# Kernel optimization log

Hardware: AMD Instinct MI355X
Metric: run time of the kernel (lower is better)

Reference implementation:

```python
import jax, jax.numpy as jnp
import numpy as np
import math

B, S, D, H = 2, 2048, 1024, 16
DH = D // H  # head_dim = 64


def setup_inputs() -> dict:
    key = jax.random.key(0)
    k0, k1, k2 = jax.random.split(key, 3)
    x = jax.random.normal(k0, (B, S, D), dtype=jnp.float32)
    Wi = jax.random.normal(k1, (3 * D, D), dtype=jnp.float32) * 0.02  # torch (out,in) layout
    bi = jnp.zeros((3 * D,), dtype=jnp.float32)
    Wo = jax.random.normal(k2, (D, D), dtype=jnp.float32) * 0.02
    bo = jnp.zeros((D,), dtype=jnp.float32)
    return {"x": x, "Wi": Wi, "bi": bi, "Wo": Wo, "bo": bo, "causal_mask": 1}


def reference(x, Wi, bi, Wo, bo, causal_mask):
    b, s, d = x.shape
    # fused QKV projection: nn.Linear applies x @ W.T + b
    qkv = x @ Wi.T + bi                      # (b, s, 3d)
    q, k, v = jnp.split(qkv, 3, axis=-1)
    # (b, s, d) -> (b, h, s, dh)
    def to_heads(t):
        return t.reshape(b, s, H, DH).transpose(0, 2, 1, 3)
    q, k, v = to_heads(q), to_heads(k), to_heads(v)
    scores = jnp.einsum("bhqd,bhkd->bhqk", q, k)  # (b, h, s, s)
    if causal_mask:
        # mask strictly-upper triangle with -inf BEFORE scaling (as in source; -inf unaffected)
        tri = jnp.triu(jnp.ones((s, s), dtype=bool), k=1)
        scores = jnp.where(tri, -jnp.inf, scores)
    scores = scores / math.sqrt(DH)
    weight = jax.nn.softmax(scores, axis=-1)
    out = jnp.einsum("bhqk,bhkd->bhqd", weight, v)  # (b, h, s, dh)
    out = out.transpose(0, 2, 1, 3).reshape(b, s, d)
    return out @ Wo.T + bo
```

## Files before the change

### kernel.cpp

```cpp
#include <hip/hip_runtime.h>
#include <hip/hip_bf16.h>
#include <stdint.h>

#define B_    2
#define S_    2048
#define D_    1024
#define H_    16
#define DH_   64
#define MTOT  (B_*S_)
#define NQKV  (3*D_)

typedef __attribute__((ext_vector_type(8))) short  bf16x8;
typedef __attribute__((ext_vector_type(4))) short  bf16x4;
typedef __attribute__((ext_vector_type(4))) float  f32x4;
typedef __attribute__((ext_vector_type(8))) unsigned short u16x8;
typedef unsigned short ushort_t;

__device__ __forceinline__ ushort_t f2bf(float f) {
  union { float f; unsigned int i; } v; v.f = f;
  unsigned int r = v.i + 0x7FFF + ((v.i >> 16) & 1);
  return (ushort_t)(r >> 16);
}

__device__ __forceinline__ unsigned cvt_pk_bf16(float lo, float hi) {
  unsigned r;
  asm("v_cvt_pk_bf16_f32 %0, %1, %2" : "=v"(r) : "v"(lo), "v"(hi));
  return r;
}

__device__ __forceinline__ float fexp2(float x) {
  float r;
  asm("v_exp_f32 %0, %1" : "=v"(r) : "v"(x));
  return r;
}

#if __has_builtin(__builtin_amdgcn_mfma_f32_16x16x16_bf16)
__device__ __forceinline__ f32x4 mfma16(bf16x4 a, bf16x4 b, f32x4 c) {
  return __builtin_amdgcn_mfma_f32_16x16x16_bf16(a, b, c, 0, 0, 0);
}
#elif __has_builtin(__builtin_amdgcn_mfma_f32_16x16x16bf16_1k)
__device__ __forceinline__ f32x4 mfma16(bf16x4 a, bf16x4 b, f32x4 c) {
  return __builtin_amdgcn_mfma_f32_16x16x16bf16_1k(a, b, c, 0, 0, 0);
}
#else
__device__ __forceinline__ f32x4 mfma16(bf16x4 a, bf16x4 b, f32x4 c) {
  asm volatile("v_mfma_f32_16x16x16_bf16 %0, %1, %2, %0"
               : "+v"(c) : "v"(a), "v"(b));
  return c;
}
#endif

__device__ __forceinline__ void gl_lds16(const ushort_t* g, ushort_t* l) {
  __builtin_amdgcn_global_load_lds(
      (const __attribute__((address_space(1))) unsigned int*)g,
      (__attribute__((address_space(3))) unsigned int*)l, 16, 0, 0);
}

#define CVN1 (MTOT*D_/8)
#define CVN2 (NQKV*D_/8)
#define CVN3 (D_*D_/8)
__global__ __launch_bounds__(256) void cvt_all(
    const float* __restrict__ x, const float* __restrict__ Wi, const float* __restrict__ Wo,
    ushort_t* __restrict__ xb, ushort_t* __restrict__ Wib, ushort_t* __restrict__ Wob) {
  int i = blockIdx.x * blockDim.x + threadIdx.x;
  const float* src; ushort_t* dst; int k;
  if (i < CVN1)            { src = x;  dst = xb;  k = i; }
  else if (i < CVN1+CVN2)  { src = Wi; dst = Wib; k = i - CVN1; }
  else                     { src = Wo; dst = Wob; k = i - CVN1 - CVN2; }
  const float4* s4 = (const float4*)src;
  float4 a = s4[2*k], b = s4[2*k+1];
  u16x8 o;
  o[0]=f2bf(a.x); o[1]=f2bf(a.y); o[2]=f2bf(a.z); o[3]=f2bf(a.w);
  o[4]=f2bf(b.x); o[5]=f2bf(b.y); o[6]=f2bf(b.z); o[7]=f2bf(b.w);
  ((u16x8*)dst)[k] = o;
}

#define BKQ 32
#define BKO 64
#define QSCALE 0.18033688011112042f
__global__ __launch_bounds__(256) void gemm_qkv(
    const ushort_t* __restrict__ Abf, const ushort_t* __restrict__ Bbf,
    const float* __restrict__ bias,
    ushort_t* __restrict__ qb, ushort_t* __restrict__ kb, ushort_t* __restrict__ vb) {
  __shared__ __align__(16) ushort_t Al[128*BKQ];
  __shared__ __align__(16) ushort_t Bl[128*BKQ];
  int tid = threadIdx.x;
  int w = tid >> 6, lane = tid & 63;
  int wrow = (w >> 1) * 64, wcol = (w & 1) * 64;
  int m0 = blockIdx.y * 128, n0 = blockIdx.x * 128;
  const int K = D_;
  f32x4 zero = {0.f, 0.f, 0.f, 0.f};
  f32x4 acc[4][4];
  for (int i=0;i<4;i++) for (int j=0;j<4;j++) acc[i][j] = zero;

  for (int k0 = 0; k0 < K; k0 += BKQ) {
    __syncthreads();
    for (int it = 0; it < 2; ++it) {
      int c = it*256 + tid;
      int row = c >> 2, cc = c & 3;
      int lbase = (it*256 + w*64) * 8;
      gl_lds16(Abf + (size_t)(m0+row)*K + k0 + cc*8, Al + lbase);
      gl_lds16(Bbf + (size_t)(n0+row)*K + k0 + cc*8, Bl + lbase);
    }
    asm volatile("s_waitcnt vmcnt(0)" ::: "memory");
    __syncthreads();
    int kof = (lane >> 4) * 8;
    bf16x8 af[4], bfr[4];
    for (int i=0;i<4;i++) af[i]  = *(const bf16x8*)(Al + (wrow + i*16 + (lane&15))*BKQ + kof);
    for (int j=0;j<4;j++) bfr[j] = *(const bf16x8*)(Bl + (wcol + j*16 + (lane&15))*BKQ + kof);
    for (int i=0;i<4;i++)
      for (int j=0;j<4;j++)
        acc[i][j] = __builtin_amdgcn_mfma_f32_16x16x32_bf16(af[i], bfr[j], acc[i][j], 0, 0, 0);
  }
  for (int i=0;i<4;i++)
    for (int j=0;j<4;j++)
      for (int r=0;r<4;r++) {
        int gm = m0 + wrow + i*16 + (lane>>4)*4 + r;
        int gn = n0 + wcol + j*16 + (lane&15);
        float v = acc[i][j][r] + bias[gn];
        int b = gm >> 11, s = gm & (S_-1);
        int sect = gn >> 10, hn = gn & (D_-1);
        int hh = hn >> 6, d = hn & 63;
        size_t idx = (((size_t)(b*H_ + hh))*S_ + s)*DH_ + d;
        if (sect == 0) v *= QSCALE;
        ushort_t val = f2bf(v);
        if (sect == 0) qb[idx] = val;
        else if (sect == 1) kb[idx] = val;
        else vb[idx] = val;
      }
}

__global__ __launch_bounds__(256) void transpose_v(
    const ushort_t* __restrict__ vb, ushort_t* __restrict__ vtb) {
  __shared__ ushort_t T[64*72];
  int bh = blockIdx.y;
  int s0 = blockIdx.x * 64;
  int tid = threadIdx.x;
  const ushort_t* src = vb + (size_t)bh * S_ * DH_;
  ushort_t* dst = vtb + (size_t)bh * DH_ * S_;
  for (int it = 0; it < 2; ++it) {
    int c = it*256 + tid;
    int row = c >> 3, cc = c & 7;
    *(uint4*)&T[row*72 + cc*8] = *(const uint4*)(src + (size_t)(s0+row)*DH_ + cc*8);
  }
  __syncthreads();
  for (int it = 0; it < 2; ++it) {
    int c = it*256 + tid;
    int d = c >> 3, sc = c & 7;
    u16x8 o;
    #pragma unroll
    for (int e = 0; e < 8; ++e) o[e] = T[(sc*8+e)*72 + d];
    *(u16x8*)(dst + (size_t)d*S_ + s0 + sc*8) = o;
  }
}

#define KVB 64
#define DTHR 8.0f
__global__ __launch_bounds__(256) void attn_fwd(
    const ushort_t* __restrict__ qb, const ushort_t* __restrict__ kb,
    const ushort_t* __restrict__ vtb, ushort_t* __restrict__ attnb,
    const int* __restrict__ causal) {
  int wg = blockIdx.x;
  int xcd = wg & 7;
  int rest = wg >> 3;
  int bh = (rest & 3) * 8 + xcd;
  int qblk = 31 - (rest >> 2);
  int b = bh >> 4, h = bh & 15;
  int tid = threadIdx.x, w = tid >> 6, lane = tid & 63;
  int g = lane >> 4, q16 = lane & 15;
  const ushort_t* qh  = qb  + (size_t)bh * S_ * DH_;
  const ushort_t* kh  = kb  + (size_t)bh * S_ * DH_;
  const ushort_t* vth = vtb + (size_t)bh * DH_ * S_;
  __shared__ __align__(16) ushort_t Kl[3][KVB*64];
  __shared__ __align__(16) ushort_t Vtl[3][64*KVB];
  bool use_causal = (causal[0] != 0);

  int nkv = use_causal ? (qblk + 1) : (S_/KVB);
  int qw = qblk*64 + w*16;

  bf16x8 qc0 = *(const bf16x8*)(qh + (size_t)(qw + q16)*DH_ +  0 + g*8);
  bf16x8 qc1 = *(const bf16x8*)(qh + (size_t)(qw + q16)*DH_ + 32 + g*8);

  int c0 = tid, c1 = tid + 256;
  int r0 = c0 >> 3, sw0 = ((c0 & 7) ^ (r0 & 7)) * 8;
  int r1 = c1 >> 3, sw1 = ((c1 & 7) ^ (r1 & 7)) * 8;
  const ushort_t* kp0 = kh + r0*DH_ + sw0;
  const ushort_t* kp1 = kh + r1*DH_ + sw1;
  const ushort_t* vp0 = vth + (size_t)r0*S_ + sw0;
  const ushort_t* vp1 = vth + (size_t)r1*S_ + sw1;

  auto stage = [&](int t, int buf) {
    size_t kadv = (size_t)(t*KVB) * DH_;
    int vadv = t*KVB;
    gl_lds16(kp0 + kadv, &Kl[buf][c0*8]);
    gl_lds16(kp1 + kadv, &Kl[buf][c1*8]);
    gl_lds16(vp0 + vadv, &Vtl[buf][c0*8]);
    gl_lds16(vp1 + vadv, &Vtl[buf][c1*8]);
  };

  f32x4 zero = {0.f,0.f,0.f,0.f};
  f32x4 o[4];
  #pragma unroll
  for (int dt=0;dt<4;dt++) o[dt] = zero;
  float mrun = -1e30f, lrun = 0.f;

  stage(0, 0);
  stage(1, 1);
  asm volatile("s_waitcnt vmcnt(4)" ::: "memory");
  __builtin_amdgcn_s_barrier();

  for (int it = 0; it < nkv; ++it) {
    int cur = it % 3;
    int kvbase = it * KVB;
    if (it + 2 < nkv) stage(it + 2, (it + 2) % 3);

    f32x4 sacc[4];
    #pragma unroll
    for (int j=0;j<4;j++) sacc[j] = zero;
    __builtin_amdgcn_s_setprio(1);
    #pragma unroll
    for (int kk=0;kk<2;kk++) {
      bf16x8 qf = kk ? qc1 : qc0;
      #pragma unroll
      for (int j=0;j<4;j++) {
        int row = j*16 + q16;
        int slot = (kk*4 + g) ^ (row & 7);
        bf16x8 kf = *(const bf16x8*)(&Kl[cur][row*64 + slot*8]);
        sacc[j] = __builtin_amdgcn_mfma_f32_16x16x32_bf16(kf, qf, sacc[j], 0, 0, 0);
      }
    }
    __builtin_amdgcn_s_setprio(0);
    if (use_causal && kvbase + KVB - 1 > qw) {
      int qd = qw + q16 - kvbase;
      #pragma unroll
      for (int j=0;j<4;j++)
        #pragma unroll
        for (int r=0;r<4;r++)
          if (16*j + 4*g + r > qd) sacc[j][r] = -1e30f;
    }
    float m0v = fmaxf(fmaxf(sacc[0][0], sacc[0][1]), fmaxf(sacc[0][2], sacc[0][3]));
    float m1v = fmaxf(fmaxf(sacc[1][0], sacc[1][1]), fmaxf(sacc[1][2], sacc[1][3]));
    float m2v = fmaxf(fmaxf(sacc[2][0], sacc[2][1]), fmaxf(sacc[2][2], sacc[2][3]));
    float m3v = fmaxf(fmaxf(sacc[3][0], sacc[3][1]), fmaxf(sacc[3][2], sacc[3][3]));
    float mx = fmaxf(fmaxf(m0v, m1v), fmaxf(m2v, m3v));
    mx = fmaxf(mx, __shfl_xor(mx, 16, 64));
    mx = fmaxf(mx, __shfl_xor(mx, 32, 64));
    if (!__all(mx - mrun <= DTHR)) {
      float mnew = fmaxf(mrun, mx);
      float alpha = fexp2(mrun - mnew);
      lrun *= alpha;
      float av0 = __shfl(alpha, 4*g + 0, 64);
      float av1 = __shfl(alpha, 4*g + 1, 64);
      float av2 = __shfl(alpha, 4*g + 2, 64);
      float av3 = __shfl(alpha, 4*g + 3, 64);
      #pragma unroll
      for (int dt=0;dt<4;dt++) {
        o[dt][0] *= av0; o[dt][1] *= av1; o[dt][2] *= av2; o[dt][3] *= av3;
      }
      mrun = mnew;
    }
    float p[4][4];
    float rs = 0.f;
    #pragma unroll
    for (int j=0;j<4;j++)
      #pragma unroll
      for (int r=0;r<4;r++) {
        p[j][r] = fexp2(sacc[j][r] - mrun);
        rs += p[j][r];
      }
    rs += __shfl_xor(rs, 16, 64);
    rs += __shfl_xor(rs, 32, 64);
    lrun += rs;
    __builtin_amdgcn_s_setprio(1);
    #pragma unroll
    for (int s=0;s<4;s++) {
      union { unsigned u[2]; bf16x4 v; } pk;
      pk.u[0] = cvt_pk_bf16(p[s][0], p[s][1]);
      pk.u[1] = cvt_pk_bf16(p[s][2], p[s][3]);
      int E = 16*s + 4*g;
      #pragma unroll
      for (int dt=0;dt<4;dt++) {
        int row = dt*16 + q16;
        int off = row*64 + ((E >> 3) ^ (row & 7))*8 + (E & 7);
        bf16x4 vf = *(const bf16x4*)(&Vtl[cur][off]);
        o[dt] = mfma16(pk.v, vf, o[dt]);
      }
    }
    __builtin_amdgcn_s_setprio(0);
    if (it + 2 < nkv) {
      asm volatile("s_waitcnt vmcnt(4)" ::: "memory");
    } else {
      asm volatile("s_waitcnt vmcnt(0)" ::: "memory");
    }
    __builtin_amdgcn_s_barrier();
  }
  float li0 = 1.f / __shfl(lrun, 4*g + 0, 64);
  float li1 = 1.f / __shfl(lrun, 4*g + 1, 64);
  float li2 = 1.f / __shfl(lrun, 4*g + 2, 64);
  float li3 = 1.f / __shfl(lrun, 4*g + 3, 64);
  #pragma unroll
  for (int r=0;r<4;r++) {
    float li = (r==0)?li0:(r==1)?li1:(r==2)?li2:li3;
    int q = qw + 4*g + r;
    #pragma unroll
    for (int dt=0;dt<4;dt++) {
      int d = dt*16 + q16;
      attnb[((size_t)(b*S_ + q))*D_ + h*DH_ + d] = f2bf(o[dt][r] * li);
    }
  }
}

__global__ __launch_bounds__(512) void gemm_out(
    const ushort_t* __restrict__ Abf, const ushort_t* __restrict__ Bbf,
    const float* __restrict__ bias, float* __restrict__ out) {
  __shared__ __align__(16) ushort_t Al[128*BKO];
  __shared__ __align__(16) ushort_t Bl[128*BKO];
  int tid = threadIdx.x;
  int w = tid >> 6, lane = tid & 63;
  int g = lane >> 4, q16 = lane & 15;
  int wrow = (w >> 2) * 64, wcol = (w & 3) * 32;
  int m0 = blockIdx.y * 128, n0 = blockIdx.x * 128;
  const int K = D_;
  f32x4 zero = {0.f,0.f,0.f,0.f};
  f32x4 acc[4][2];
  for (int i=0;i<4;i++) for (int j=0;j<2;j++) acc[i][j] = zero;

  for (int k0 = 0; k0 < K; k0 += BKO) {
    __syncthreads();
    #pragma unroll
    for (int it = 0; it < 2; ++it) {
      int c = it*512 + tid;
      int row = c >> 3, scc = ((c & 7) ^ (row & 7)) * 8;
      gl_lds16(Abf + (size_t)(m0+row)*K + k0 + scc, Al + c*8);
      gl_lds16(Bbf + (size_t)(n0+row)*K + k0 + scc, Bl + c*8);
    }
    asm volatile("s_waitcnt vmcnt(0)" ::: "memory");
    __syncthreads();
    #pragma unroll
    for (int kk = 0; kk < 2; ++kk) {
      bf16x8 af[4], bfr[2];
      #pragma unroll
      for (int i=0;i<4;i++) {
        int row = wrow + i*16 + q16;
        int slot = ((kk*4 + g) ^ (row & 7)) * 8;
        af[i] = *(const bf16x8*)(Al + row*BKO + slot);
      }
      #pragma unroll
      for (int j=0;j<2;j++) {
        int row = wcol + j*16 + q16;
        int slot = ((kk*4 + g) ^ (row & 7)) * 8;
        bfr[j] = *(const bf16x8*)(Bl + row*BKO + slot);
      }
      #pragma unroll
      for (int i=0;i<4;i++)
        #pragma unroll
        for (int j=0;j<2;j++)
          acc[i][j] = __builtin_amdgcn_mfma_f32_16x16x32_bf16(af[i], bfr[j], acc[i][j], 0, 0, 0);
    }
  }
  #pragma unroll
  for (int i=0;i<4;i++)
    #pragma unroll
    for (int j=0;j<2;j++)
      #pragma unroll
      for (int r=0;r<4;r++) {
        int gm = m0 + wrow + i*16 + g*4 + r;
        int gn = n0 + wcol + j*16 + q16;
        out[(size_t)gm*D_ + gn] = acc[i][j][r] + bias[gn];
      }
}

extern "C" void kernel_launch(void* const* d_in, const int* in_sizes, int n_in,
                              void* d_out, int out_size, void* d_ws, size_t ws_size,
                              hipStream_t stream) {
  const float* x  = (const float*)d_in[0];
  const float* Wi = (const float*)d_in[1];
  const float* bi = (const float*)d_in[2];
  const float* Wo = (const float*)d_in[3];
  const float* bo = (const float*)d_in[4];
  const int* causal = (const int*)d_in[5];
  float* out = (float*)d_out;

  ushort_t* xb   = (ushort_t*)d_ws;
  ushort_t* Wib  = xb  + (size_t)MTOT*D_;
  ushort_t* Wob  = Wib + (size_t)NQKV*D_;
  ushort_t* qbuf = Wob + (size_t)D_*D_;
  ushort_t* kbuf = qbuf + (size_t)B_*H_*S_*DH_;
  ushort_t* vbuf = kbuf + (size_t)B_*H_*S_*DH_;
  ushort_t* attnb = vbuf + (size_t)B_*H_*S_*DH_;
  ushort_t* vtb  = xb;

  int ntot = CVN1 + CVN2 + CVN3;
  cvt_all<<<(ntot+255)/256, 256, 0, stream>>>(x, Wi, Wo, xb, Wib, Wob);

  gemm_qkv<<<dim3(NQKV/128, MTOT/128), 256, 0, stream>>>(xb, Wib, bi, qbuf, kbuf, vbuf);
  transpose_v<<<dim3(S_/64, B_*H_), 256, 0, stream>>>(vbuf, vtb);
  attn_fwd<<<1024, 256, 0, stream>>>(qbuf, kbuf, vtb, attnb, causal);
  gemm_out<<<dim3(D_/128, MTOT/128), 512, 0, stream>>>(attnb, Wob, bo, out);
}
```

Before: 122.4 us.

## Switch attention to double buffering with serpentine q-block scheduling, drop setprio

The attention kernel goes from a 3-stage to a 2-stage LDS pipeline, which halves the LDS footprint so more workgroups can fit per CU, at the cost of less prefetch lookahead. The workgroup-to-q-block mapping changes to a serpentine order, alternating heavy and light causal blocks within each group of eight to balance load across the wave of dispatch. The s_setprio hints around the MFMA sections are removed. Several inner loop variables are renamed to avoid clashing with the new index variables.

```diff
diff --git a/kernel.cpp b/kernel.cpp
--- a/kernel.cpp
+++ b/kernel.cpp
@@ -162,17 +162,21 @@
     const int* __restrict__ causal) {
   int wg = blockIdx.x;
   int xcd = wg & 7;
-  int rest = wg >> 3;
-  int bh = (rest & 3) * 8 + xcd;
-  int qblk = 31 - (rest >> 2);
+  int j = wg >> 3;
+  int v = j >> 5;
+  int u = j & 31;
+  int a = u >> 2;
+  int qi = v*8 + ((v & 1) ? (7 - a) : a);
+  int qblk = 31 - qi;
+  int bh = (u & 3) * 8 + xcd;
   int b = bh >> 4, h = bh & 15;
   int tid = threadIdx.x, w = tid >> 6, lane = tid & 63;
   int g = lane >> 4, q16 = lane & 15;
   const ushort_t* qh  = qb  + (size_t)bh * S_ * DH_;
   const ushort_t* kh  = kb  + (size_t)bh * S_ * DH_;
   const ushort_t* vth = vtb + (size_t)bh * DH_ * S_;
-  __shared__ __align__(16) ushort_t Kl[3][KVB*64];
-  __shared__ __align__(16) ushort_t Vtl[3][64*KVB];
+  __shared__ __align__(16) ushort_t Kl[2][KVB*64];
+  __shared__ __align__(16) ushort_t Vtl[2][64*KVB];
   bool use_causal = (causal[0] != 0);
 
   int nkv = use_causal ? (qblk + 1) : (S_/KVB);
@@ -205,38 +209,35 @@
   float mrun = -1e30f, lrun = 0.f;
 
   stage(0, 0);
-  stage(1, 1);
-  asm volatile("s_waitcnt vmcnt(4)" ::: "memory");
+  asm volatile("s_waitcnt vmcnt(0)" ::: "memory");
   __builtin_amdgcn_s_barrier();
 
   for (int it = 0; it < nkv; ++it) {
-    int cur = it % 3;
+    int cur = it & 1;
     int kvbase = it * KVB;
-    if (it + 2 < nkv) stage(it + 2, (it + 2) % 3);
+    if (it + 1 < nkv) stage(it + 1, cur ^ 1);
 
     f32x4 sacc[4];
     #pragma unroll
-    for (int j=0;j<4;j++) sacc[j] = zero;
-    __builtin_amdgcn_s_setprio(1);
+    for (int j2=0;j2<4;j2++) sacc[j2] = zero;
     #pragma unroll
     for (int kk=0;kk<2;kk++) {
       bf16x8 qf = kk ? qc1 : qc0;
       #pragma unroll
-      for (int j=0;j<4;j++) {
-        int row = j*16 + q16;
+      for (int j2=0;j2<4;j2++) {
+        int row = j2*16 + q16;
         int slot = (kk*4 + g) ^ (row & 7);
         bf16x8 kf = *(const bf16x8*)(&Kl[cur][row*64 + slot*8]);
-        sacc[j] = __builtin_amdgcn_mfma_f32_16x16x32_bf16(kf, qf, sacc[j], 0, 0, 0);
-      }
-    }
-    __builtin_amdgcn_s_setprio(0);
+        sacc[j2] = __builtin_amdgcn_mfma_f32_16x16x32_bf16(kf, qf, sacc[j2], 0, 0, 0);
+      }
+    }
     if (use_causal && kvbase + KVB - 1 > qw) {
       int qd = qw + q16 - kvbase;
       #pragma unroll
-      for (int j=0;j<4;j++)
+      for (int j2=0;j2<4;j2++)
         #pragma unroll
         for (int r=0;r<4;r++)
-          if (16*j + 4*g + r > qd) sacc[j][r] = -1e30f;
+          if (16*j2 + 4*g + r > qd) sacc[j2][r] = -1e30f;
     }
     float m0v = fmaxf(fmaxf(sacc[0][0], sacc[0][1]), fmaxf(sacc[0][2], sacc[0][3]));
     float m1v = fmaxf(fmaxf(sacc[1][0], sacc[1][1]), fmaxf(sacc[1][2], sacc[1][3]));
@@ -262,36 +263,30 @@
     float p[4][4];
     float rs = 0.f;
     #pragma unroll
-    for (int j=0;j<4;j++)
+    for (int j2=0;j2<4;j2++)
       #pragma unroll
       for (int r=0;r<4;r++) {
-        p[j][r] = fexp2(sacc[j][r] - mrun);
-        rs += p[j][r];
+        p[j2][r] = fexp2(sacc[j2][r] - mrun);
+        rs += p[j2][r];
       }
     rs += __shfl_xor(rs, 16, 64);
     rs += __shfl_xor(rs, 32, 64);
     lrun += rs;
-    __builtin_amdgcn_s_setprio(1);
     #pragma unroll
     for (int s=0;s<4;s++) {
-      union { unsigned u[2]; bf16x4 v; } pk;
-      pk.u[0] = cvt_pk_bf16(p[s][0], p[s][1]);
-      pk.u[1] = cvt_pk_bf16(p[s][2], p[s][3]);
+      union { unsigned u2[2]; bf16x4 v2; } pk;
+      pk.u2[0] = cvt_pk_bf16(p[s][0], p[s][1]);
+      pk.u2[1] = cvt_pk_bf16(p[s][2], p[s][3]);
       int E = 16*s + 4*g;
       #pragma unroll
       for (int dt=0;dt<4;dt++) {
         int row = dt*16 + q16;
         int off = row*64 + ((E >> 3) ^ (row & 7))*8 + (E & 7);
         bf16x4 vf = *(const bf16x4*)(&Vtl[cur][off]);
-        o[dt] = mfma16(pk.v, vf, o[dt]);
-      }
-    }
-    __builtin_amdgcn_s_setprio(0);
-    if (it + 2 < nkv) {
-      asm volatile("s_waitcnt vmcnt(4)" ::: "memory");
-    } else {
-      asm volatile("s_waitcnt vmcnt(0)" ::: "memory");
-    }
+        o[dt] = mfma16(pk.v2, vf, o[dt]);
+      }
+    }
+    asm volatile("s_waitcnt vmcnt(0)" ::: "memory");
     __builtin_amdgcn_s_barrier();
   }
   float li0 = 1.f / __shfl(lrun, 4*g + 0, 64);
```

Measured after the change: 120.0 us. About the same (-1.9%).
